# Optimization experiments

Measured on AMD Instinct MI355X. Metric: run time of the kernel, lower is better.

## Reference

```python
import jax, jax.numpy as jnp
import numpy as np

# 2D-LSTM wavefront recurrence (Bahar et al. 2018). Cell: gates i,f,o,lambda (sigmoid)
# and candidate g (tanh) from affine([x_cat; s_hor; s_ver]);
# c = f*(lam*c_hor + (1-lam)*c_ver) + i*g ; s = o*tanh(c).
# Returns full hidden-state grid states_s[1:,1:,:,:] reshaped to [I, O, B, H].

B, I, O, F, H = 64, 48, 48, 256, 256


def setup_inputs() -> dict:
    key = jax.random.key(0)
    k0, k1, k2, k3 = jax.random.split(key, 4)
    scale = 1.0 / np.sqrt(2 * F + 2 * H)
    return {
        "x": jax.random.normal(k0, (B, I, F), jnp.float32),
        "y": jax.random.normal(k1, (B, O, F), jnp.float32),
        "Wx": jax.random.normal(k2, (2 * F, 5 * H), jnp.float32) * scale,
        "Ws": jax.random.normal(k3, (2 * H, 5 * H), jnp.float32) * scale,
        "b": jnp.zeros((5 * H,), jnp.float32),
    }


def reference(x, y, Wx, Ws, b):
    Bn, In, Fn = x.shape
    On = y.shape[1]
    Hn = Ws.shape[0] // 2
    xT = jnp.transpose(x, (1, 0, 2))  # [I, B, F]
    yT = jnp.transpose(y, (1, 0, 2))  # [O, B, F]
    i_idx = jnp.arange(In)
    n_diag = In + On - 1

    def shift_down(a):  # lane i reads lane i-1 (zeros at i=0) -> horizontal predecessor
        return jnp.concatenate([jnp.zeros_like(a[:1]), a[:-1]], axis=0)

    def step(carry, d):
        s_buf, c_buf = carry  # [I, B, H]: states of diagonal d-1, keyed by input index i
        j = d - i_idx  # output index per lane on diagonal d
        valid = (j >= 0) & (j < On)
        s_hor, c_hor = shift_down(s_buf), shift_down(c_buf)  # cell (i-1, j)
        vmask = (j >= 1)[:, None, None]
        s_ver = jnp.where(vmask, s_buf, 0.0)  # cell (i, j-1)
        c_ver = jnp.where(vmask, c_buf, 0.0)
        y_cur = yT[jnp.clip(j, 0, On - 1)]  # [I, B, F]
        inp = jnp.concatenate([xT, y_cur], axis=-1)  # [I, B, 2F]
        st = jnp.concatenate([s_hor, s_ver], axis=-1)  # [I, B, 2H]
        pre = inp @ Wx + st @ Ws + b  # [I, B, 5H]
        ig, fg, og, lg, gg = jnp.split(pre, 5, axis=-1)
        ig, fg = jax.nn.sigmoid(ig), jax.nn.sigmoid(fg)
        og, lg = jax.nn.sigmoid(og), jax.nn.sigmoid(lg)
        gg = jnp.tanh(gg)
        c_next = fg * (lg * c_hor + (1.0 - lg) * c_ver) + ig * gg
        s_next = og * jnp.tanh(c_next)
        m = valid[:, None, None]
        s_new = jnp.where(m, s_next, 0.0)
        c_new = jnp.where(m, c_next, 0.0)
        return (s_new, c_new), s_new

    init = (jnp.zeros((In, Bn, Hn), x.dtype), jnp.zeros((In, Bn, Hn), x.dtype))
    _, ys = jax.lax.scan(step, init, jnp.arange(n_diag))  # [n_diag, I, B, H]
    ii = jnp.arange(In)[:, None]
    jj = jnp.arange(On)[None, :]
    grid = ys[ii + jj, ii]  # [I, O, B, H] : hidden state of every 2D cell
    return grid
```

## Files before the change

kernel.cpp:

```cpp
#include <hip/hip_runtime.h>
#include <hip/hip_bf16.h>

typedef __attribute__((ext_vector_type(8))) short short8;
typedef __attribute__((ext_vector_type(4))) float floatx4;

#define Bb 64
#define Ii 48
#define Oo 48
#define Ff 256
#define Hh 256
#define NG 1280
#define KK 512
#define CHUNK 80
#define NH 16
#define HCHUNKS 16
#define WORKERS 16
#define RING 4
#define WLDS_STRIDE 520
#define WLDS_STRIDE_PRE 264
#define DSTRIDE 84

__global__ __launch_bounds__(256) void pack_kernel(
    const float* __restrict__ Wx, const float* __restrict__ Ws,
    const float* __restrict__ x, const float* __restrict__ y,
    __hip_bfloat16* __restrict__ Wxp, __hip_bfloat16* __restrict__ Wsp,
    __hip_bfloat16* __restrict__ xb, __hip_bfloat16* __restrict__ yb) {
  int idx = blockIdx.x * blockDim.x + threadIdx.x;
  int stride = gridDim.x * blockDim.x;
  int total_w = NG * KK;
  for (int t = idx; t < total_w; t += stride) {
    int np = t / KK, k = t % KK;
    int orig = (np % 5) * Hh + (np / 5);
    Wxp[t] = __float2bfloat16(Wx[k * NG + orig]);
    Wsp[t] = __float2bfloat16(Ws[k * NG + orig]);
  }
  int total_x = Bb * Ii * Ff;
  for (int t = idx; t < total_x; t += stride) {
    int f = t % Ff; int rest = t / Ff; int b = rest % Bb; int i = rest / Bb;
    xb[(i * Bb + b) * Ff + f] = __float2bfloat16(x[(b * Ii + i) * Ff + f]);
    yb[(i * Bb + b) * Ff + f] = __float2bfloat16(y[(b * Oo + i) * Ff + f]);
  }
}

__global__ __launch_bounds__(256) void pregemm(
    const __hip_bfloat16* __restrict__ xb, const __hip_bfloat16* __restrict__ yb,
    const __hip_bfloat16* __restrict__ Wxp,
    float* __restrict__ Px, float* __restrict__ Py) {
  __shared__ __hip_bfloat16 Wl[CHUNK * WLDS_STRIDE_PRE];
  int wg = blockIdx.x;
  int isY = wg >= (Ii * HCHUNKS);
  int w = isY ? wg - Ii * HCHUNKS : wg;
  int mblk = w >> 4;
  int hc = w & 15;
  int n0 = hc * CHUNK;
  int koff = isY ? Ff : 0;
  int tid = threadIdx.x;
  for (int idx = tid; idx < CHUNK * (Ff / 8); idx += 256) {
    int cl = idx >> 5;
    int kb = (idx & 31) << 3;
    *(short8*)&Wl[cl * WLDS_STRIDE_PRE + kb] =
        *(const short8*)&Wxp[(n0 + cl) * KK + koff + kb];
  }
  __syncthreads();
  int wave = tid >> 6, lane = tid & 63;
  int lr = lane & 15, q = lane >> 4;
  const __hip_bfloat16* Arow = (isY ? yb : xb) + ((size_t)mblk * Bb + wave * 16 + lr) * Ff;
  floatx4 acc[5];
#pragma unroll
  for (int t = 0; t < 5; t++) acc[t] = (floatx4){0.f, 0.f, 0.f, 0.f};
#pragma unroll
  for (int ks = 0; ks < Ff / 32; ks++) {
    int k = ks * 32 + q * 8;
    short8 a = *(const short8*)(Arow + k);
#pragma unroll
    for (int t = 0; t < 5; t++) {
      short8 bfr = *(const short8*)&Wl[(t * 16 + lr) * WLDS_STRIDE_PRE + k];
      acc[t] = __builtin_amdgcn_mfma_f32_16x16x32_bf16(a, bfr, acc[t], 0, 0, 0);
    }
  }
  float* Pr = (isY ? Py : Px) + (size_t)mblk * Bb * NG + n0;
#pragma unroll
  for (int t = 0; t < 5; t++)
#pragma unroll
    for (int r = 0; r < 4; r++)
      Pr[(wave * 16 + q * 4 + r) * NG + t * 16 + lr] = acc[t][r];
}

__device__ __forceinline__ void wait16(const int* p) {
  while (__hip_atomic_load(p, __ATOMIC_RELAXED, __HIP_MEMORY_SCOPE_AGENT) < HCHUNKS)
    __builtin_amdgcn_s_sleep(1);
}

__device__ __forceinline__ short8 load8_sc(const __hip_bfloat16* p) {
  const unsigned long long* q = (const unsigned long long*)p;
  union { unsigned long long u[2]; short8 v; } r;
  r.u[0] = __hip_atomic_load(q,     __ATOMIC_RELAXED, __HIP_MEMORY_SCOPE_AGENT);
  r.u[1] = __hip_atomic_load(q + 1, __ATOMIC_RELAXED, __HIP_MEMORY_SCOPE_AGENT);
  return r.v;
}

__device__ __forceinline__ void store_bf16_sc(__hip_bfloat16* p, float f) {
  union { __hip_bfloat16 b; unsigned short u; } cv;
  cv.b = __float2bfloat16(f);
  __hip_atomic_store((unsigned short*)p, cv.u, __ATOMIC_RELAXED, __HIP_MEMORY_SCOPE_AGENT);
}

__global__ __launch_bounds__(256) void lstm_row(
    const float* __restrict__ Px, const float* __restrict__ Py,
    const float* __restrict__ bias, const __hip_bfloat16* __restrict__ Wsp,
    __hip_bfloat16* __restrict__ Sring, float* __restrict__ Cring,
    const __hip_bfloat16* __restrict__ Szero,
    float* __restrict__ out, int* __restrict__ done) {
  __shared__ __hip_bfloat16 Wl[CHUNK * WLDS_STRIDE];
  __shared__ float Dl[Bb * DSTRIDE];
  __shared__ float Pxl[Bb * DSTRIDE];
  int wg = blockIdx.x;
  int worker = wg >> 4;
  int hc = wg & 15;
  int n0 = hc * CHUNK;
  int h0 = hc * NH;
  int tid = threadIdx.x;
  int wave = tid >> 6, lane = tid & 63;
  int lr = lane & 15, q = lane >> 4;
  int hl = tid & 15;
  int brow0 = tid >> 4;

  for (int idx = tid; idx < CHUNK * (KK / 8); idx += 256) {
    int cl = idx >> 6;
    int kb = (idx & 63) << 3;
    *(short8*)&Wl[cl * WLDS_STRIDE + kb] = *(const short8*)&Wsp[(n0 + cl) * KK + kb];
  }
  float bv[5];
#pragma unroll
  for (int g = 0; g < 5; g++) bv[g] = bias[g * Hh + h0 + hl];

#pragma unroll 1
  for (int rr = 0; rr < 3; rr++) {
    int i = worker + rr * WORKERS;
    for (int idx = tid; idx < Bb * CHUNK; idx += 256) {
      int b = idx / CHUNK, c = idx - b * CHUNK;
      Pxl[b * DSTRIDE + c] = Px[(size_t)i * Bb * NG + b * NG + n0 + c];
    }
    float cvreg[4];
#pragma unroll
    for (int it = 0; it < 4; it++) cvreg[it] = 0.f;

#pragma unroll 1
    for (int j = 0; j < Oo; j++) {
      const float* PyR = Py + (size_t)j * Bb * NG + n0;
      float pyv[4][5];
#pragma unroll
      for (int it = 0; it < 4; it++) {
        int base = (brow0 + 16 * it) * NG + 5 * hl;
#pragma unroll
        for (int g = 0; g < 5; g++) pyv[it][g] = PyR[base + g];
      }
      if (tid == 0) {
        if (i > 0) wait16(done + (i - 1) * Oo + j);
        if (j > 0) wait16(done + i * Oo + (j - 1));
        if (i + 1 < Ii && j >= RING) wait16(done + (i + 1) * Oo + (j - RING));
      }
      __syncthreads();

      const __hip_bfloat16* Sv = (i > 0)
          ? Sring + ((size_t)(i - 1) * RING + (j & (RING - 1))) * (Bb * Hh) : Szero;
      const __hip_bfloat16* Sh = (j > 0)
          ? Sring + ((size_t)i * RING + ((j - 1) & (RING - 1))) * (Bb * Hh) : Szero;
      __hip_bfloat16* Sout = Sring + ((size_t)i * RING + (j & (RING - 1))) * (Bb * Hh);
      float* Cout = Cring + ((size_t)i * RING + (j & (RING - 1))) * (Bb * Hh);

      float chv[4];
      if (i > 0) {
        const float* Chp = Cring + ((size_t)(i - 1) * RING + (j & (RING - 1))) * (Bb * Hh);
#pragma unroll
        for (int it = 0; it < 4; it++)
          chv[it] = __hip_atomic_load(&Chp[(brow0 + 16 * it) * Hh + h0 + hl],
                                      __ATOMIC_RELAXED, __HIP_MEMORY_SCOPE_AGENT);
      } else {
#pragma unroll
        for (int it = 0; it < 4; it++) chv[it] = 0.f;
      }

      const __hip_bfloat16* SvR = Sv + (size_t)(wave * 16 + lr) * Hh;
      const __hip_bfloat16* ShR = Sh + (size_t)(wave * 16 + lr) * Hh;
      floatx4 acc[5];
#pragma unroll
      for (int t = 0; t < 5; t++) acc[t] = (floatx4){0.f, 0.f, 0.f, 0.f};
#pragma unroll
      for (int ks = 0; ks < KK / 32; ks++) {
        int k = ks * 32 + q * 8;
        short8 a = (k < Hh) ? load8_sc(SvR + k) : load8_sc(ShR + (k - Hh));
#pragma unroll
        for (int t = 0; t < 5; t++) {
          short8 bfr = *(const short8*)&Wl[(t * 16 + lr) * WLDS_STRIDE + k];
          acc[t] = __builtin_amdgcn_mfma_f32_16x16x32_bf16(a, bfr, acc[t], 0, 0, 0);
        }
      }
#pragma unroll
      for (int t = 0; t < 5; t++)
#pragma unroll
        for (int r = 0; r < 4; r++)
          Dl[(wave * 16 + q * 4 + r) * DSTRIDE + t * 16 + lr] = acc[t][r];
      __syncthreads();
#pragma unroll
      for (int it = 0; it < 4; it++) {
        int b = brow0 + 16 * it;
        float pre[5];
#pragma unroll
        for (int g = 0; g < 5; g++)
          pre[g] = Dl[b * DSTRIDE + 5 * hl + g] + Pxl[b * DSTRIDE + 5 * hl + g]
                 + pyv[it][g] + bv[g];
        float ig = 1.f / (1.f + __expf(-pre[0]));
        float fg = 1.f / (1.f + __expf(-pre[1]));
        float og = 1.f / (1.f + __expf(-pre[2]));
        float lg = 1.f / (1.f + __expf(-pre[3]));
        float gg = 1.f - 2.f / (__expf(2.f * pre[4]) + 1.f);
        float cn = fg * (lg * chv[it] + (1.f - lg) * cvreg[it]) + ig * gg;
        float tc = 1.f - 2.f / (__expf(2.f * cn) + 1.f);
        float sn = og * tc;
        cvreg[it] = cn;
        int h = h0 + hl;
        __hip_atomic_store(&Cout[b * Hh + h], cn,
                           __ATOMIC_RELAXED, __HIP_MEMORY_SCOPE_AGENT);
        store_bf16_sc(&Sout[b * Hh + h], sn);
        out[(((size_t)i * Oo + j) * Bb + b) * Hh + h] = sn;
      }
      __syncthreads();
      if (tid == 0) atomicAdd(done + i * Oo + j, 1);
    }
  }
}

extern "C" void kernel_launch(void* const* d_in, const int* in_sizes, int n_in,
                              void* d_out, int out_size, void* d_ws, size_t ws_size,
                              hipStream_t stream) {
  const float* x    = (const float*)d_in[0];
  const float* y    = (const float*)d_in[1];
  const float* Wx   = (const float*)d_in[2];
  const float* Ws   = (const float*)d_in[3];
  const float* bias = (const float*)d_in[4];
  float* out = (float*)d_out;

  char* ws = (char*)d_ws;
  size_t off = 0;
  auto alloc = [&](size_t bytes) -> void* {
    void* p = ws + off;
    off += (bytes + 255) & ~(size_t)255;
    return p;
  };
  __hip_bfloat16* Wxp = (__hip_bfloat16*)alloc((size_t)NG * KK * 2);
  __hip_bfloat16* Wsp = (__hip_bfloat16*)alloc((size_t)NG * KK * 2);
  __hip_bfloat16* xb  = (__hip_bfloat16*)alloc((size_t)Ii * Bb * Ff * 2);
  __hip_bfloat16* yb  = (__hip_bfloat16*)alloc((size_t)Oo * Bb * Ff * 2);
  float* Px = (float*)alloc((size_t)Ii * Bb * NG * 4);
  float* Py = (float*)alloc((size_t)Oo * Bb * NG * 4);
  __hip_bfloat16* Sring = (__hip_bfloat16*)alloc((size_t)Ii * RING * Bb * Hh * 2);
  float* Cring = (float*)alloc((size_t)Ii * RING * Bb * Hh * 4);
  char* zbase = ws + off;
  __hip_bfloat16* Szero = (__hip_bfloat16*)alloc((size_t)Bb * Hh * 2);
  int*   done = (int*)alloc((size_t)Ii * Oo * 4);
  size_t zBytes = (size_t)((ws + off) - zbase);

  hipMemsetAsync(zbase, 0, zBytes, stream);

  hipLaunchKernelGGL(pack_kernel, dim3(512), dim3(256), 0, stream,
                     Wx, Ws, x, y, Wxp, Wsp, xb, yb);
  hipLaunchKernelGGL(pregemm, dim3(2 * Ii * HCHUNKS), dim3(256), 0, stream,
                     xb, yb, Wxp, Px, Py);

  void* args[] = {(void*)&Px, (void*)&Py, (void*)&bias, (void*)&Wsp,
                  (void*)&Sring, (void*)&Cring, (void*)&Szero,
                  (void*)&out, (void*)&done};
  hipLaunchCooperativeKernel((void*)lstm_row, dim3(WORKERS * HCHUNKS), dim3(256),
                             args, 0, stream);
}
```

Baseline: 1.709 ms.

## Permute gate columns so MFMA accumulators feed the LSTM epilogue directly

Weight packing now orders columns per chunk as gate-major blocks of 16 hidden units, so each MFMA tile holds one gate for 16 hidden units. The epilogue then reads gate pre-activations straight from the accumulator registers instead of staging them through an LDS tile and a barrier. Px is likewise held in registers rather than LDS. This takes an LDS round trip and a __syncthreads off the serial per-step critical path. In exchange, Py/Px loads become strided column gathers and register pressure goes up.

```diff
diff --git a/kernel.cpp b/kernel.cpp
--- a/kernel.cpp
+++ b/kernel.cpp
@@ -18,7 +18,6 @@
 #define RING 4
 #define WLDS_STRIDE 520
 #define WLDS_STRIDE_PRE 264
-#define DSTRIDE 84
 
 __global__ __launch_bounds__(256) void pack_kernel(
     const float* __restrict__ Wx, const float* __restrict__ Ws,
@@ -30,7 +29,11 @@
   int total_w = NG * KK;
   for (int t = idx; t < total_w; t += stride) {
     int np = t / KK, k = t % KK;
-    int orig = (np % 5) * Hh + (np / 5);
+    int hcp = np / CHUNK;
+    int rem = np - hcp * CHUNK;
+    int g = rem >> 4;
+    int hsub = rem & 15;
+    int orig = g * Hh + hcp * NH + hsub;
     Wxp[t] = __float2bfloat16(Wx[k * NG + orig]);
     Wsp[t] = __float2bfloat16(Ws[k * NG + orig]);
   }
@@ -112,8 +115,6 @@
     const __hip_bfloat16* __restrict__ Szero,
     float* __restrict__ out, int* __restrict__ done) {
   __shared__ __hip_bfloat16 Wl[CHUNK * WLDS_STRIDE];
-  __shared__ float Dl[Bb * DSTRIDE];
-  __shared__ float Pxl[Bb * DSTRIDE];
   int wg = blockIdx.x;
   int worker = wg >> 4;
   int hc = wg & 15;
@@ -122,8 +123,9 @@
   int tid = threadIdx.x;
   int wave = tid >> 6, lane = tid & 63;
   int lr = lane & 15, q = lane >> 4;
-  int hl = tid & 15;
-  int brow0 = tid >> 4;
+  const int brow = wave * 16 + q * 4;
+  const int hme = h0 + lr;
+  const size_t BH = (size_t)Bb * Hh;
 
   for (int idx = tid; idx < CHUNK * (KK / 8); idx += 256) {
     int cl = idx >> 6;
@@ -132,15 +134,18 @@
   }
   float bv[5];
 #pragma unroll
-  for (int g = 0; g < 5; g++) bv[g] = bias[g * Hh + h0 + hl];
+  for (int g = 0; g < 5; g++) bv[g] = bias[g * Hh + hme];
 
 #pragma unroll 1
   for (int rr = 0; rr < 3; rr++) {
     int i = worker + rr * WORKERS;
-    for (int idx = tid; idx < Bb * CHUNK; idx += 256) {
-      int b = idx / CHUNK, c = idx - b * CHUNK;
-      Pxl[b * DSTRIDE + c] = Px[(size_t)i * Bb * NG + b * NG + n0 + c];
-    }
+    float pxv[4][5];
+#pragma unroll
+    for (int ra = 0; ra < 4; ra++)
+#pragma unroll
+      for (int g = 0; g < 5; g++)
+        pxv[ra][g] = Px[((size_t)i * Bb + (brow + ra)) * NG + n0 + g * 16 + lr];
+
     float cvreg[4];
 #pragma unroll
     for (int it = 0; it < 4; it++) cvreg[it] = 0.f;
@@ -150,11 +155,11 @@
       const float* PyR = Py + (size_t)j * Bb * NG + n0;
       float pyv[4][5];
 #pragma unroll
-      for (int it = 0; it < 4; it++) {
-        int base = (brow0 + 16 * it) * NG + 5 * hl;
-#pragma unroll
-        for (int g = 0; g < 5; g++) pyv[it][g] = PyR[base + g];
-      }
+      for (int ra = 0; ra < 4; ra++)
+#pragma unroll
+        for (int g = 0; g < 5; g++)
+          pyv[ra][g] = PyR[(size_t)(brow + ra) * NG + g * 16 + lr];
+
       if (tid == 0) {
         if (i > 0) wait16(done + (i - 1) * Oo + j);
         if (j > 0) wait16(done + i * Oo + (j - 1));
@@ -163,22 +168,22 @@
       __syncthreads();
 
       const __hip_bfloat16* Sv = (i > 0)
-          ? Sring + ((size_t)(i - 1) * RING + (j & (RING - 1))) * (Bb * Hh) : Szero;
+          ? Sring + ((size_t)(i - 1) * RING + (j & (RING - 1))) * BH : Szero;
       const __hip_bfloat16* Sh = (j > 0)
-          ? Sring + ((size_t)i * RING + ((j - 1) & (RING - 1))) * (Bb * Hh) : Szero;
-      __hip_bfloat16* Sout = Sring + ((size_t)i * RING + (j & (RING - 1))) * (Bb * Hh);
-      float* Cout = Cring + ((size_t)i * RING + (j & (RING - 1))) * (Bb * Hh);
+          ? Sring + ((size_t)i * RING + ((j - 1) & (RING - 1))) * BH : Szero;
+      __hip_bfloat16* Sout = Sring + ((size_t)i * RING + (j & (RING - 1))) * BH;
+      float* Cout = Cring + ((size_t)i * RING + (j & (RING - 1))) * BH;
 
       float chv[4];
       if (i > 0) {
-        const float* Chp = Cring + ((size_t)(i - 1) * RING + (j & (RING - 1))) * (Bb * Hh);
-#pragma unroll
-        for (int it = 0; it < 4; it++)
-          chv[it] = __hip_atomic_load(&Chp[(brow0 + 16 * it) * Hh + h0 + hl],
+        const float* Chp = Cring + ((size_t)(i - 1) * RING + (j & (RING - 1))) * BH;
+#pragma unroll
+        for (int ra = 0; ra < 4; ra++)
+          chv[ra] = __hip_atomic_load(&Chp[(size_t)(brow + ra) * Hh + hme],
                                       __ATOMIC_RELAXED, __HIP_MEMORY_SCOPE_AGENT);
       } else {
 #pragma unroll
-        for (int it = 0; it < 4; it++) chv[it] = 0.f;
+        for (int ra = 0; ra < 4; ra++) chv[ra] = 0.f;
       }
 
       const __hip_bfloat16* SvR = Sv + (size_t)(wave * 16 + lr) * Hh;
@@ -196,34 +201,27 @@
           acc[t] = __builtin_amdgcn_mfma_f32_16x16x32_bf16(a, bfr, acc[t], 0, 0, 0);
         }
       }
-#pragma unroll
-      for (int t = 0; t < 5; t++)
-#pragma unroll
-        for (int r = 0; r < 4; r++)
-          Dl[(wave * 16 + q * 4 + r) * DSTRIDE + t * 16 + lr] = acc[t][r];
-      __syncthreads();
-#pragma unroll
-      for (int it = 0; it < 4; it++) {
-        int b = brow0 + 16 * it;
+
+#pragma unroll
+      for (int ra = 0; ra < 4; ra++) {
+        int b = brow + ra;
         float pre[5];
 #pragma unroll
         for (int g = 0; g < 5; g++)
-          pre[g] = Dl[b * DSTRIDE + 5 * hl + g] + Pxl[b * DSTRIDE + 5 * hl + g]
-                 + pyv[it][g] + bv[g];
+          pre[g] = acc[g][ra] + pxv[ra][g] + pyv[ra][g] + bv[g];
         float ig = 1.f / (1.f + __expf(-pre[0]));
         float fg = 1.f / (1.f + __expf(-pre[1]));
         float og = 1.f / (1.f + __expf(-pre[2]));
         float lg = 1.f / (1.f + __expf(-pre[3]));
         float gg = 1.f - 2.f / (__expf(2.f * pre[4]) + 1.f);
-        float cn = fg * (lg * chv[it] + (1.f - lg) * cvreg[it]) + ig * gg;
+        float cn = fg * (lg * chv[ra] + (1.f - lg) * cvreg[ra]) + ig * gg;
         float tc = 1.f - 2.f / (__expf(2.f * cn) + 1.f);
         float sn = og * tc;
-        cvreg[it] = cn;
-        int h = h0 + hl;
-        __hip_atomic_store(&Cout[b * Hh + h], cn,
+        cvreg[ra] = cn;
+        __hip_atomic_store(&Cout[(size_t)b * Hh + hme], cn,
                            __ATOMIC_RELAXED, __HIP_MEMORY_SCOPE_AGENT);
-        store_bf16_sc(&Sout[b * Hh + h], sn);
-        out[(((size_t)i * Oo + j) * Bb + b) * Hh + h] = sn;
+        store_bf16_sc(&Sout[(size_t)b * Hh + hme], sn);
+        out[(((size_t)i * Oo + j) * Bb + b) * Hh + hme] = sn;
       }
       __syncthreads();
       if (tid == 0) atomicAdd(done + i * Oo + j, 1);
```

Measured after the change: 1.591 ms. -6.9%, faster.
